# Optimization experiments

Measured on AMD Instinct MI355X. Metric: run time of the kernel, lower is better.

## Reference

```python
import jax, jax.numpy as jnp
import numpy as np

N = 100_000      # nodes
E = 800_000      # edges (avg degree 8)
IN = 64          # in_channels
OUT = 64         # out_channels
HEADS = 4
HD = OUT // HEADS  # per-head out channels (concat=True)


def _unif(key, shape, fan_in):
    b = 1.0 / np.sqrt(fan_in)
    return jax.random.uniform(key, shape, jnp.float32, -b, b)


def setup_inputs() -> dict:
    key = jax.random.key(0)
    ks = jax.random.split(key, 12)
    x = jax.random.normal(ks[0], (N, IN), jnp.float32)
    pos = jax.random.normal(ks[1], (N, 3), jnp.float32)
    edge_index = jax.random.randint(ks[2], (2, E), 0, N, jnp.int32)
    # Per-head PointTransformerConv params (stacked over heads).
    # lin / lin_src / lin_dst are bias-free Linear(in, hd); pos_nn is Linear(3, hd) with bias.
    W_lin = _unif(ks[3], (HEADS, IN, HD), IN)
    W_src = _unif(ks[4], (HEADS, IN, HD), IN)
    W_dst = _unif(ks[5], (HEADS, IN, HD), IN)
    W_pos = _unif(ks[6], (HEADS, 3, HD), 3)
    b_pos = _unif(ks[7], (HEADS, HD), 3)
    # projection MLP: Linear(OUT,OUT) -> ReLU -> Linear(OUT,OUT)
    W1 = _unif(ks[8], (OUT, OUT), OUT)
    b1 = _unif(ks[9], (OUT,), OUT)
    W2 = _unif(ks[10], (OUT, OUT), OUT)
    b2 = _unif(ks[11], (OUT,), OUT)
    return dict(x=x, pos=pos, edge_index=edge_index, W_lin=W_lin, W_src=W_src,
                W_dst=W_dst, W_pos=W_pos, b_pos=b_pos, W1=W1, b1=b1, W2=W2, b2=b2)


def reference(x, pos, edge_index, W_lin, W_src, W_dst, W_pos, b_pos, W1, b1, W2, b2):
    # Add self-loops (PointTransformerConv default add_self_loops=True).
    loops = jnp.arange(N, dtype=edge_index.dtype)
    src = jnp.concatenate([edge_index[0], loops])   # j (source)
    dst = jnp.concatenate([edge_index[1], loops])   # i (target)

    # Per-node, all-heads projections: [N, H, HD]
    v = jnp.einsum('ni,hio->nho', x, W_lin)
    a_src = jnp.einsum('ni,hio->nho', x, W_src)
    a_dst = jnp.einsum('ni,hio->nho', x, W_dst)

    # Relative-position encoding delta = pos_nn(pos_i - pos_j): [Et, H, HD]
    rel = pos[dst] - pos[src]
    delta = jnp.einsum('ec,hco->eho', rel, W_pos) + b_pos

    # Attention logits per edge/channel: alpha_i - alpha_j + delta
    alpha = a_dst[dst] - a_src[src] + delta

    # Segment softmax over incoming edges of each target node (numerically stable).
    amax = jax.ops.segment_max(alpha, dst, num_segments=N)
    amax = jnp.where(jnp.isfinite(amax), amax, 0.0)
    ex = jnp.exp(alpha - amax[dst])
    denom = jax.ops.segment_sum(ex, dst, num_segments=N)
    attn = ex / jnp.maximum(denom[dst], 1e-16)

    # Message = attn * (lin(x_j) + delta), scatter-sum to targets: [N, H, HD]
    msg = attn * (v[src] + delta)
    out_h = jax.ops.segment_sum(msg, dst, num_segments=N)

    # Concat heads -> projection MLP
    out = out_h.reshape(N, HEADS * HD)
    h = jax.nn.relu(out @ W1 + b1)
    return h @ W2 + b2
```

## Files before the change

### kernel.cpp

```cpp
#include <hip/hip_runtime.h>
#include <math.h>


typedef _Float16 f16;
typedef _Float16 f16x2 __attribute__((ext_vector_type(2)));
typedef _Float16 f16x4 __attribute__((ext_vector_type(4)));
typedef _Float16 f16x8 __attribute__((ext_vector_type(8)));
typedef float f32x4 __attribute__((ext_vector_type(4)));

#define A_PITCH 104
#define C_PITCH 136
#define LOG2E 1.44269504f
#define S_CAP 32

__global__ __launch_bounds__(256) void zero_wprep_kernel(
    int Zb, int* __restrict__ cnt, int N,
    const float* __restrict__ Ws, const float* __restrict__ Wl,
    const float* __restrict__ Wp,
    const float* __restrict__ W1, const float* __restrict__ W2,
    f16* __restrict__ Bt, f16* __restrict__ W1p, f16* __restrict__ W2p)
{
    if ((int)blockIdx.x < Zb) {
        int i4 = (blockIdx.x * 256 + threadIdx.x) * 4;
        if (i4 + 3 < N) {
            *(int4*)&cnt[i4] = make_int4(0, 0, 0, 0);
        } else {
            for (int i = i4; i < N; i++) cnt[i] = 0;
        }
        return;
    }
    int idx = (blockIdx.x - Zb) * 256 + threadIdx.x;
    if (idx < 128 * 96) {
        int col = idx / 96, k = idx - col * 96;
        float v = 0.f;
        int p = col >> 1, h = p >> 4, o = p & 15;
        if (col & 1) {
            if (k < 64)      v = Wl[h * 1024 + k * 16 + o];
            else if (k < 67) v = -Wp[h * 48 + (k - 64) * 16 + o];
        } else {
            if (k < 64)      v = -LOG2E * Ws[h * 1024 + k * 16 + o];
            else if (k < 67) v = -LOG2E * Wp[h * 48 + (k - 64) * 16 + o];
        }
        Bt[col * 96 + k] = (f16)v;
    } else if (idx < 128 * 96 + 4096) {
        int t = idx - 128 * 96;
        int col = t >> 6, k = t & 63;
        W1p[col * 64 + k] = (f16)W1[k * 64 + col];
    } else if (idx < 128 * 96 + 8192) {
        int t = idx - 128 * 96 - 4096;
        int col = t >> 6, k = t & 63;
        W2p[col * 64 + k] = (f16)W2[k * 64 + col];
    }
}

__global__ __launch_bounds__(256) void gemm_hist_kernel(
    const float* __restrict__ x, const float* __restrict__ pos,
    const f16* __restrict__ Bt,
    f16* __restrict__ AV, int N, int Gb,
    const int* __restrict__ ei, int E, int Hb4,
    int* __restrict__ cnt, int* __restrict__ ssrc)
{
    __shared__ f16 smem[64 * C_PITCH];
    int tid = threadIdx.x;

    if (blockIdx.x & 1) {
        int hb = blockIdx.x >> 1;
        if (hb >= Hb4) return;
        int chunk = hb >> 2, cls = hb & 3;
        int e0 = chunk * 512 + tid;
        int e1 = e0 + 256;
        int d0 = 0, d1 = 0;
        bool a0 = e0 < E, a1 = e1 < E;
        if (a0) d0 = ei[E + e0];
        if (a1) d1 = ei[E + e1];
        bool k0 = a0 && ((d0 & 3) == cls);
        bool k1 = a1 && ((d1 & 3) == cls);
        int s0 = 0, s1 = 0;
        if (k0) s0 = ei[e0];
        if (k1) s1 = ei[e1];
        if (k0) {
            int r = atomicAdd(&cnt[d0], 1);
            if (r < S_CAP) ssrc[d0 * S_CAP + r] = s0;
        }
        if (k1) {
            int r = atomicAdd(&cnt[d1], 1);
            if (r < S_CAP) ssrc[d1 * S_CAP + r] = s1;
        }
        return;
    }

    int gb = blockIdx.x >> 1;
    if (gb >= Gb) return;
    int l = tid & 63, wv = tid >> 6;
    int quad = l >> 4, lr = l & 15;
    int nb = gb * 64;

    for (int it = 0; it < 4; it++) {
        int q = it * 256 + tid;
        int n = q >> 4, k = (q & 15) * 4;
        float4 xv = make_float4(0.f, 0.f, 0.f, 0.f);
        if (nb + n < N) xv = *(const float4*)&x[(size_t)(nb + n) * 64 + k];
        f16x4 h4; h4[0] = (f16)xv.x; h4[1] = (f16)xv.y; h4[2] = (f16)xv.z; h4[3] = (f16)xv.w;
        *(f16x4*)&smem[n * A_PITCH + k] = h4;
    }
    {
        int n = tid >> 2, seg = tid & 3;
        f16x4 z = {(f16)0, (f16)0, (f16)0, (f16)0};
        f16x4 h4 = z;
        if (seg == 0 && nb + n < N) {
            h4[0] = (f16)pos[(size_t)(nb + n) * 3 + 0];
            h4[1] = (f16)pos[(size_t)(nb + n) * 3 + 1];
            h4[2] = (f16)pos[(size_t)(nb + n) * 3 + 2];
            h4[3] = (f16)1.0f;
        }
        *(f16x4*)&smem[n * A_PITCH + 64 + seg * 8] = h4;
        *(f16x4*)&smem[n * A_PITCH + 64 + seg * 8 + 4] = z;
    }
    __syncthreads();

    f16x8 af[4][3];
    #pragma unroll
    for (int mt = 0; mt < 4; mt++)
        #pragma unroll
        for (int kt = 0; kt < 3; kt++)
            af[mt][kt] = *(const f16x8*)&smem[(mt * 16 + lr) * A_PITCH + kt * 32 + quad * 8];
    __syncthreads();

    #pragma unroll
    for (int t = 0; t < 2; t++) {
        int colBase = (wv * 2 + t) * 16;
        f16x8 b0 = *(const f16x8*)&Bt[(colBase + lr) * 96 + 0  + quad * 8];
        f16x8 b1 = *(const f16x8*)&Bt[(colBase + lr) * 96 + 32 + quad * 8];
        f16x8 b2 = *(const f16x8*)&Bt[(colBase + lr) * 96 + 64 + quad * 8];
        #pragma unroll
        for (int mt = 0; mt < 4; mt++) {
            f32x4 acc = {0.f, 0.f, 0.f, 0.f};
            acc = __builtin_amdgcn_mfma_f32_16x16x32_f16(af[mt][0], b0, acc, 0, 0, 0);
            acc = __builtin_amdgcn_mfma_f32_16x16x32_f16(af[mt][1], b1, acc, 0, 0, 0);
            acc = __builtin_amdgcn_mfma_f32_16x16x32_f16(af[mt][2], b2, acc, 0, 0, 0);
            int col = colBase + lr;
            #pragma unroll
            for (int r = 0; r < 4; r++) {
                int row = mt * 16 + quad * 4 + r;
                smem[row * C_PITCH + col] = (f16)acc[r];
            }
        }
    }
    __syncthreads();

    for (int it = 0; it < 4; it++) {
        int cid = it * 256 + tid;
        int row = cid >> 4, off = (cid & 15) * 8;
        if (nb + row < N) {
            f16x8 w8 = *(const f16x8*)&smem[row * C_PITCH + off];
            f16x8 o;
            #pragma unroll
            for (int p = 0; p < 4; p++) {
                float e  = __builtin_amdgcn_exp2f((float)w8[2 * p]);
                float ev = e * (float)w8[2 * p + 1];
                o[2 * p]     = (f16)e;
                o[2 * p + 1] = (f16)ev;
            }
            *(f16x8*)&AV[(size_t)(nb + row) * 128 + off] = o;
        }
    }
}

__global__ __launch_bounds__(256) void attn_mlp_kernel(
    const f16* __restrict__ AV,
    const int* __restrict__ cnt, const int* __restrict__ ssrc,
    const float* __restrict__ pos, const float* __restrict__ Wp,
    const float* __restrict__ bp,
    const f16* __restrict__ W1p, const f16* __restrict__ W2p,
    const float* __restrict__ b1, const float* __restrict__ b2,
    float* __restrict__ out, int N)
{
    __shared__ f16 As[32 * 72];
    __shared__ f16 Hs[32 * 72];
    int tid = threadIdx.x, c = tid & 63, wv = tid >> 6;
    int quad = c >> 4, lr = c & 15;
    int nb = blockIdx.x * 32;

    float wpx = Wp[quad * 48 + 0  + lr];
    float wpy = Wp[quad * 48 + 16 + lr];
    float wpz = Wp[quad * 48 + 32 + lr];
    float bpc = bp[c];

    const f16x2* AV2 = (const f16x2*)AV;

    for (int pt = 0; pt < 4; pt++) {
        int i0 = __builtin_amdgcn_readfirstlane(nb + wv * 8 + pt * 2);
        int i1 = i0 + 1;
        if (i1 >= N) i1 = N - 1;
        if (i0 >= N) i0 = N - 1;
        int deg0 = __builtin_amdgcn_readfirstlane(cnt[i0]); if (deg0 > S_CAP) deg0 = S_CAP;
        int deg1 = __builtin_amdgcn_readfirstlane(cnt[i1]); if (deg1 > S_CAP) deg1 = S_CAP;
        float Gi0 = pos[i0 * 3 + 0] * wpx + pos[i0 * 3 + 1] * wpy + pos[i0 * 3 + 2] * wpz + bpc;
        float Gi1 = pos[i1 * 3 + 0] * wpx + pos[i1 * 3 + 1] * wpy + pos[i1 * 3 + 2] * wpz + bpc;
        f16x2 sv0 = AV2[(size_t)i0 * 64 + c];
        f16x2 sv1 = AV2[(size_t)i1 * 64 + c];
        float den0 = (float)sv0[0], num0 = (float)sv0[1];
        float den1 = (float)sv1[0], num1 = (float)sv1[1];
        int base0 = i0 * S_CAP, base1 = i1 * S_CAP;

        for (int b = 0; b < S_CAP; b += 8) {
            bool r0 = b < deg0, r1 = b < deg1;
            if (!(r0 | r1)) break;
            f16x2 w0[8], w1[8];
            if (r0) {
                #pragma unroll
                for (int s = 0; s < 8; s++) {
                    int jj = __builtin_amdgcn_readfirstlane(ssrc[base0 + b + s]);
                    if ((b + s) >= deg0 || (unsigned)jj >= (unsigned)N) jj = 0;
                    w0[s] = AV2[(size_t)jj * 64 + c];
                }
            }
            if (r1) {
                #pragma unroll
                for (int s = 0; s < 8; s++) {
                    int jj = __builtin_amdgcn_readfirstlane(ssrc[base1 + b + s]);
                    if ((b + s) >= deg1 || (unsigned)jj >= (unsigned)N) jj = 0;
                    w1[s] = AV2[(size_t)jj * 64 + c];
                }
            }
            if (r0) {
                #pragma unroll
                for (int s = 0; s < 8; s++) {
                    bool ok = (b + s) < deg0;
                    den0 += ok ? (float)w0[s][0] : 0.f;
                    num0 += ok ? (float)w0[s][1] : 0.f;
                }
            }
            if (r1) {
                #pragma unroll
                for (int s = 0; s < 8; s++) {
                    bool ok = (b + s) < deg1;
                    den1 += ok ? (float)w1[s][0] : 0.f;
                    num1 += ok ? (float)w1[s][1] : 0.f;
                }
            }
        }
        As[(wv * 8 + pt * 2) * 72 + c]     = (f16)(num0 / den0 + Gi0);
        As[(wv * 8 + pt * 2 + 1) * 72 + c] = (f16)(num1 / den1 + Gi1);
    }
    __syncthreads();

    f16x8 af[2][2];
    #pragma unroll
    for (int mt = 0; mt < 2; mt++)
        #pragma unroll
        for (int kt = 0; kt < 2; kt++)
            af[mt][kt] = *(const f16x8*)&As[(mt * 16 + lr) * 72 + kt * 32 + quad * 8];

    int col = wv * 16 + lr;
    f16x8 wb0 = *(const f16x8*)&W1p[col * 64 + quad * 8];
    f16x8 wb1 = *(const f16x8*)&W1p[col * 64 + 32 + quad * 8];
    float bias1 = b1[col];
    #pragma unroll
    for (int mt = 0; mt < 2; mt++) {
        f32x4 acc = {0.f, 0.f, 0.f, 0.f};
        acc = __builtin_amdgcn_mfma_f32_16x16x32_f16(af[mt][0], wb0, acc, 0, 0, 0);
        acc = __builtin_amdgcn_mfma_f32_16x16x32_f16(af[mt][1], wb1, acc, 0, 0, 0);
        #pragma unroll
        for (int r = 0; r < 4; r++) {
            int row = mt * 16 + quad * 4 + r;
            Hs[row * 72 + col] = (f16)fmaxf(acc[r] + bias1, 0.f);
        }
    }
    __syncthreads();

    f16x8 ag[2][2];
    #pragma unroll
    for (int mt = 0; mt < 2; mt++)
        #pragma unroll
        for (int kt = 0; kt < 2; kt++)
            ag[mt][kt] = *(const f16x8*)&Hs[(mt * 16 + lr) * 72 + kt * 32 + quad * 8];

    f16x8 wc0 = *(const f16x8*)&W2p[col * 64 + quad * 8];
    f16x8 wc1 = *(const f16x8*)&W2p[col * 64 + 32 + quad * 8];
    float bias2 = b2[col];
    #pragma unroll
    for (int mt = 0; mt < 2; mt++) {
        f32x4 acc = {0.f, 0.f, 0.f, 0.f};
        acc = __builtin_amdgcn_mfma_f32_16x16x32_f16(ag[mt][0], wc0, acc, 0, 0, 0);
        acc = __builtin_amdgcn_mfma_f32_16x16x32_f16(ag[mt][1], wc1, acc, 0, 0, 0);
        #pragma unroll
        for (int r = 0; r < 4; r++) {
            int row = nb + mt * 16 + quad * 4 + r;
            if (row < N) out[(size_t)row * 64 + col] = acc[r] + bias2;
        }
    }
}

extern "C" void kernel_launch(void* const* d_in, const int* in_sizes, int n_in,
                              void* d_out, int out_size, void* d_ws, size_t ws_size,
                              hipStream_t stream)
{
    const float* x    = (const float*)d_in[0];
    const float* pos  = (const float*)d_in[1];
    const int*   ei   = (const int*)d_in[2];
    const float* Wl   = (const float*)d_in[3];
    const float* Ws   = (const float*)d_in[4];
    const float* Wp   = (const float*)d_in[6];
    const float* bpos = (const float*)d_in[7];
    const float* W1   = (const float*)d_in[8];
    const float* b1   = (const float*)d_in[9];
    const float* W2   = (const float*)d_in[10];
    const float* b2   = (const float*)d_in[11];
    float* out = (float*)d_out;

    const int N = in_sizes[0] / 64;
    const int E = in_sizes[2] / 2;

    char* w = (char*)d_ws;
    f16*  AV   = (f16*)w;                   w += (size_t)N * 128 * 2;
    f16*  Bt   = (f16*)w;                   w += 128 * 96 * 2;
    f16*  W1p  = (f16*)w;                   w += 4096 * 2;
    f16*  W2p  = (f16*)w;                   w += 4096 * 2;
    int*  cnt  = (int*)w;                   w += (size_t)N * 4;
    int*  ssrc = (int*)w;                   w += (size_t)N * S_CAP * 4;

    const int Zb  = (N + 1023) / 1024;
    const int Pb  = (128 * 96 + 8192 + 255) / 256;
    const int Gb  = (N + 63) / 64;
    const int Hb4 = ((E + 511) / 512) * 4;
    const int Kb  = (Gb > Hb4 ? Gb : Hb4) * 2;

    zero_wprep_kernel<<<Zb + Pb, 256, 0, stream>>>(Zb, cnt, N, Ws, Wl, Wp,
                                                   W1, W2, Bt, W1p, W2p);
    gemm_hist_kernel<<<Kb, 256, 0, stream>>>(x, pos, Bt, AV, N, Gb,
                                             ei, E, Hb4, cnt, ssrc);
    attn_mlp_kernel<<<(N + 31) / 32, 256, 0, stream>>>(AV, cnt, ssrc, pos, Wp, bpos,
                                                       W1p, W2p, b1, b2, out, N);
}
```

Measured before the change: 184.6 us.

## Batch neighbor gathers with split-wave node pairs and drop class-partitioned histogram

The edge-bucketing pass now handles each edge once, replacing four class-filtered passes over the edge list with a single pass and fewer blocks. The attention gather kernel splits each wave into two halves, one per target node, with each lane loading four f16 values. Neighbor indices are loaded as int4 vectors, and the first eight neighbors of all four node pairs are gathered up front to raise memory-level parallelism. This trades higher register pressure and more concurrent atomics on the count array for fewer dependent, serialized gather rounds.

```diff
diff --git a/kernel.cpp b/kernel.cpp
--- a/kernel.cpp
+++ b/kernel.cpp
@@ -57,7 +57,7 @@
     const float* __restrict__ x, const float* __restrict__ pos,
     const f16* __restrict__ Bt,
     f16* __restrict__ AV, int N, int Gb,
-    const int* __restrict__ ei, int E, int Hb4,
+    const int* __restrict__ ei, int E, int Hb2,
     int* __restrict__ cnt, int* __restrict__ ssrc)
 {
     __shared__ f16 smem[64 * C_PITCH];
@@ -65,24 +65,18 @@
 
     if (blockIdx.x & 1) {
         int hb = blockIdx.x >> 1;
-        if (hb >= Hb4) return;
-        int chunk = hb >> 2, cls = hb & 3;
-        int e0 = chunk * 512 + tid;
+        if (hb >= Hb2) return;
+        int e0 = hb * 512 + tid;
         int e1 = e0 + 256;
-        int d0 = 0, d1 = 0;
+        int s0 = 0, d0 = 0, s1 = 0, d1 = 0;
         bool a0 = e0 < E, a1 = e1 < E;
-        if (a0) d0 = ei[E + e0];
-        if (a1) d1 = ei[E + e1];
-        bool k0 = a0 && ((d0 & 3) == cls);
-        bool k1 = a1 && ((d1 & 3) == cls);
-        int s0 = 0, s1 = 0;
-        if (k0) s0 = ei[e0];
-        if (k1) s1 = ei[e1];
-        if (k0) {
+        if (a0) { s0 = ei[e0]; d0 = ei[E + e0]; }
+        if (a1) { s1 = ei[e1]; d1 = ei[E + e1]; }
+        if (a0) {
             int r = atomicAdd(&cnt[d0], 1);
             if (r < S_CAP) ssrc[d0 * S_CAP + r] = s0;
         }
-        if (k1) {
+        if (a1) {
             int r = atomicAdd(&cnt[d1], 1);
             if (r < S_CAP) ssrc[d1 * S_CAP + r] = s1;
         }
@@ -177,74 +171,139 @@
 {
     __shared__ f16 As[32 * 72];
     __shared__ f16 Hs[32 * 72];
-    int tid = threadIdx.x, c = tid & 63, wv = tid >> 6;
-    int quad = c >> 4, lr = c & 15;
+    int tid = threadIdx.x;
+    int lane = tid & 63, wv = tid >> 6;
+    int half = lane >> 5, l5 = lane & 31;
     int nb = blockIdx.x * 32;
 
-    float wpx = Wp[quad * 48 + 0  + lr];
-    float wpy = Wp[quad * 48 + 16 + lr];
-    float wpz = Wp[quad * 48 + 32 + lr];
-    float bpc = bp[c];
-
-    const f16x2* AV2 = (const f16x2*)AV;
-
-    for (int pt = 0; pt < 4; pt++) {
-        int i0 = __builtin_amdgcn_readfirstlane(nb + wv * 8 + pt * 2);
-        int i1 = i0 + 1;
-        if (i1 >= N) i1 = N - 1;
-        if (i0 >= N) i0 = N - 1;
-        int deg0 = __builtin_amdgcn_readfirstlane(cnt[i0]); if (deg0 > S_CAP) deg0 = S_CAP;
-        int deg1 = __builtin_amdgcn_readfirstlane(cnt[i1]); if (deg1 > S_CAP) deg1 = S_CAP;
-        float Gi0 = pos[i0 * 3 + 0] * wpx + pos[i0 * 3 + 1] * wpy + pos[i0 * 3 + 2] * wpz + bpc;
-        float Gi1 = pos[i1 * 3 + 0] * wpx + pos[i1 * 3 + 1] * wpy + pos[i1 * 3 + 2] * wpz + bpc;
-        f16x2 sv0 = AV2[(size_t)i0 * 64 + c];
-        f16x2 sv1 = AV2[(size_t)i1 * 64 + c];
-        float den0 = (float)sv0[0], num0 = (float)sv0[1];
-        float den1 = (float)sv1[0], num1 = (float)sv1[1];
-        int base0 = i0 * S_CAP, base1 = i1 * S_CAP;
-
-        for (int b = 0; b < S_CAP; b += 8) {
-            bool r0 = b < deg0, r1 = b < deg1;
-            if (!(r0 | r1)) break;
-            f16x2 w0[8], w1[8];
-            if (r0) {
+    const f16x4* AV4 = (const f16x4*)AV;
+
+    int sbase[4], gbase[4];
+    int4 jv0[4], jv1[4];
+    #pragma unroll
+    for (int d = 0; d < 4; d++) {
+        int ia = nb + wv * 8 + d * 2;
+        int ib = ia + 1;
+        if (ib >= N) ib = N - 1;
+        if (ia >= N) ia = N - 1;
+        int isel = half ? ib : ia;
+        sbase[d] = isel * S_CAP;
+        gbase[d] = isel * 32;
+        jv0[d] = *(const int4*)&ssrc[sbase[d]];
+        jv1[d] = *(const int4*)&ssrc[sbase[d] + 4];
+    }
+
+    f16x4 sv[4];
+    float px[4], py[4], pz[4];
+    int degS[4], mdeg[4];
+    #pragma unroll
+    for (int d = 0; d < 4; d++) {
+        sv[d] = AV4[(size_t)gbase[d] + l5];
+        int isel = sbase[d] / S_CAP;
+        px[d] = pos[isel * 3 + 0];
+        py[d] = pos[isel * 3 + 1];
+        pz[d] = pos[isel * 3 + 2];
+        int ia = nb + wv * 8 + d * 2;
+        int ib = ia + 1;
+        if (ib >= N) ib = N - 1;
+        if (ia >= N) ia = N - 1;
+        int dA = cnt[ia]; if (dA > S_CAP) dA = S_CAP;
+        int dB = cnt[ib]; if (dB > S_CAP) dB = S_CAP;
+        degS[d] = half ? dB : dA;
+        mdeg[d] = __builtin_amdgcn_readfirstlane(dA > dB ? dA : dB);
+    }
+
+    int c0 = l5 * 2;
+    int hh = c0 >> 4, oo = c0 & 15;
+    float wpx0 = Wp[hh * 48 +  0 + oo], wpx1 = Wp[hh * 48 +  0 + oo + 1];
+    float wpy0 = Wp[hh * 48 + 16 + oo], wpy1 = Wp[hh * 48 + 16 + oo + 1];
+    float wpz0 = Wp[hh * 48 + 32 + oo], wpz1 = Wp[hh * 48 + 32 + oo + 1];
+    float bp0 = bp[c0], bp1 = bp[c0 + 1];
+
+    f16x4 w[4][8];
+    #pragma unroll
+    for (int d = 0; d < 4; d++) {
+        int js[8] = {jv0[d].x, jv0[d].y, jv0[d].z, jv0[d].w,
+                     jv1[d].x, jv1[d].y, jv1[d].z, jv1[d].w};
+        #pragma unroll
+        for (int s = 0; s < 8; s++) {
+            int jj = js[s];
+            if ((unsigned)jj >= (unsigned)N) jj = 0;
+            w[d][s] = AV4[(size_t)jj * 32 + l5];
+        }
+    }
+
+    float dn0[4], nm0[4], dn1[4], nm1[4];
+    #pragma unroll
+    for (int d = 0; d < 4; d++) {
+        dn0[d] = (float)sv[d][0]; nm0[d] = (float)sv[d][1];
+        dn1[d] = (float)sv[d][2]; nm1[d] = (float)sv[d][3];
+        #pragma unroll
+        for (int s = 0; s < 8; s++) {
+            bool ok = s < degS[d];
+            dn0[d] += ok ? (float)w[d][s][0] : 0.f;
+            nm0[d] += ok ? (float)w[d][s][1] : 0.f;
+            dn1[d] += ok ? (float)w[d][s][2] : 0.f;
+            nm1[d] += ok ? (float)w[d][s][3] : 0.f;
+        }
+    }
+
+    int mm = mdeg[0];
+    if (mdeg[1] > mm) mm = mdeg[1];
+    if (mdeg[2] > mm) mm = mdeg[2];
+    if (mdeg[3] > mm) mm = mdeg[3];
+
+    for (int b = 8; b < S_CAP; b += 8) {
+        if (b >= mm) break;
+        int4 k0[4], k1[4];
+        #pragma unroll
+        for (int d = 0; d < 4; d++) {
+            k0[d] = *(const int4*)&ssrc[sbase[d] + b];
+            k1[d] = *(const int4*)&ssrc[sbase[d] + b + 4];
+        }
+        f16x4 w2[4][8];
+        #pragma unroll
+        for (int d = 0; d < 4; d++) {
+            if (b < mdeg[d]) {
+                int js[8] = {k0[d].x, k0[d].y, k0[d].z, k0[d].w,
+                             k1[d].x, k1[d].y, k1[d].z, k1[d].w};
                 #pragma unroll
                 for (int s = 0; s < 8; s++) {
-                    int jj = __builtin_amdgcn_readfirstlane(ssrc[base0 + b + s]);
-                    if ((b + s) >= deg0 || (unsigned)jj >= (unsigned)N) jj = 0;
-                    w0[s] = AV2[(size_t)jj * 64 + c];
+                    int jj = js[s];
+                    if ((b + s) >= degS[d] || (unsigned)jj >= (unsigned)N) jj = 0;
+                    w2[d][s] = AV4[(size_t)jj * 32 + l5];
                 }
             }
-            if (r1) {
+        }
+        #pragma unroll
+        for (int d = 0; d < 4; d++) {
+            if (b < mdeg[d]) {
                 #pragma unroll
                 for (int s = 0; s < 8; s++) {
-                    int jj = __builtin_amdgcn_readfirstlane(ssrc[base1 + b + s]);
-                    if ((b + s) >= deg1 || (unsigned)jj >= (unsigned)N) jj = 0;
-                    w1[s] = AV2[(size_t)jj * 64 + c];
+                    bool ok = (b + s) < degS[d];
+                    dn0[d] += ok ? (float)w2[d][s][0] : 0.f;
+                    nm0[d] += ok ? (float)w2[d][s][1] : 0.f;
+                    dn1[d] += ok ? (float)w2[d][s][2] : 0.f;
+                    nm1[d] += ok ? (float)w2[d][s][3] : 0.f;
                 }
             }
-            if (r0) {
-                #pragma unroll
-                for (int s = 0; s < 8; s++) {
-                    bool ok = (b + s) < deg0;
-                    den0 += ok ? (float)w0[s][0] : 0.f;
-                    num0 += ok ? (float)w0[s][1] : 0.f;
-                }
-            }
-            if (r1) {
-                #pragma unroll
-                for (int s = 0; s < 8; s++) {
-                    bool ok = (b + s) < deg1;
-                    den1 += ok ? (float)w1[s][0] : 0.f;
-                    num1 += ok ? (float)w1[s][1] : 0.f;
-                }
-            }
-        }
-        As[(wv * 8 + pt * 2) * 72 + c]     = (f16)(num0 / den0 + Gi0);
-        As[(wv * 8 + pt * 2 + 1) * 72 + c] = (f16)(num1 / den1 + Gi1);
-    }
-    __syncthreads();
-
+        }
+    }
+
+    #pragma unroll
+    for (int d = 0; d < 4; d++) {
+        float g0 = px[d] * wpx0 + py[d] * wpy0 + pz[d] * wpz0 + bp0;
+        float g1 = px[d] * wpx1 + py[d] * wpy1 + pz[d] * wpz1 + bp1;
+        f16x2 o;
+        o[0] = (f16)(nm0[d] / dn0[d] + g0);
+        o[1] = (f16)(nm1[d] / dn1[d] + g1);
+        int row = wv * 8 + d * 2 + half;
+        *(f16x2*)&As[row * 72 + c0] = o;
+    }
+    __syncthreads();
+
+    int c = tid & 63;
+    int quad = c >> 4, lr = c & 15;
     f16x8 af[2][2];
     #pragma unroll
     for (int mt = 0; mt < 2; mt++)
@@ -323,13 +382,13 @@
     const int Zb  = (N + 1023) / 1024;
     const int Pb  = (128 * 96 + 8192 + 255) / 256;
     const int Gb  = (N + 63) / 64;
-    const int Hb4 = ((E + 511) / 512) * 4;
-    const int Kb  = (Gb > Hb4 ? Gb : Hb4) * 2;
+    const int Hb2 = (E + 511) / 512;
+    const int Kb  = (Gb > Hb2 ? Gb : Hb2) * 2;
 
     zero_wprep_kernel<<<Zb + Pb, 256, 0, stream>>>(Zb, cnt, N, Ws, Wl, Wp,
                                                    W1, W2, Bt, W1p, W2p);
     gemm_hist_kernel<<<Kb, 256, 0, stream>>>(x, pos, Bt, AV, N, Gb,
-                                             ei, E, Hb4, cnt, ssrc);
+                                             ei, E, Hb2, cnt, ssrc);
     attn_mlp_kernel<<<(N + 31) / 32, 256, 0, stream>>>(AV, cnt, ssrc, pos, Wp, bpos,
                                                        W1p, W2p, b1, b2, out, N);
 }
```

After: 197.8 us. 1.07x slower.
